# Kernel optimization log

Measured on AMD Instinct MI355X. Metric: run time of the kernel, lower is better.

Reference implementation:

```python
import jax, jax.numpy as jnp
import numpy as np

B, T, V, E, H, F, L = 128, 30, 10000, 512, 512, 4096, 2


def setup_inputs() -> dict:
    key = jax.random.key(0)
    ks = jax.random.split(key, 8)
    s = lambda n: np.float32(1.0 / np.sqrt(n))
    return {
        "vgg_fc7": jax.random.normal(ks[0], (B, F), jnp.float32),
        "xTokens": jax.random.randint(ks[1], (B, T), 0, V),
        "embedding": jax.random.normal(ks[2], (V, E), jnp.float32) * 0.1,
        "W_in": jax.random.normal(ks[3], (F, H), jnp.float32) * s(F),
        "b_in": jnp.zeros((H,), jnp.float32),
        # GRU params stacked over layers; layer0 input dim E == H so shapes match
        "Wu": jax.random.normal(ks[4], (L, E + H, H), jnp.float32) * s(E + H),
        "bu": jnp.zeros((L, H), jnp.float32),
        "Wr": jax.random.normal(ks[5], (L, E + H, H), jnp.float32) * s(E + H),
        "br": jnp.zeros((L, H), jnp.float32),
        "Wc": jax.random.normal(ks[6], (L, E + H, H), jnp.float32) * s(E + H),
        "bc": jnp.zeros((L, H), jnp.float32),
        "W_out": jax.random.normal(ks[7], (H, V), jnp.float32) * s(H),
        "b_out": jnp.zeros((V,), jnp.float32),
    }


def reference(vgg_fc7, xTokens, embedding, W_in, b_in, Wu, bu, Wr, br, Wc, bc, W_out, b_out):
    # initial hidden state = tanh(inputLayer(vgg_fc7)), replicated per layer
    h0 = jnp.tanh(vgg_fc7 @ W_in + b_in)            # [B, H]
    states0 = jnp.broadcast_to(h0, (L, B, H))
    x_emb = embedding[xTokens]                      # [B, T, E]

    def step(states, x_t):
        x = x_t                                     # [B, E]
        new = []
        for j in range(L):
            h = states[j]
            conc = jnp.concatenate([x, h], axis=1)              # [B, E+H]
            u = jax.nn.sigmoid(conc @ Wu[j] + bu[j])            # update gate
            r = jax.nn.sigmoid(conc @ Wr[j] + br[j])            # reset gate
            cand = jnp.tanh(jnp.concatenate([x, r * h], axis=1) @ Wc[j] + bc[j])
            h = u * h + (1.0 - u) * cand
            new.append(h)
            x = h
        logits_t = x @ W_out + b_out                # [B, V]
        return jnp.stack(new), logits_t

    final_state, logits = jax.lax.scan(step, states0, jnp.swapaxes(x_emb, 0, 1))
    logits = jnp.swapaxes(logits, 0, 1)             # [B, T, V]
    return logits, final_state
```

## Files before the change

kernel.cpp:

```cpp
#include <hip/hip_runtime.h>
#include <hip/hip_bf16.h>

#define B_   128
#define T_   30
#define V_   10000
#define E_   512
#define H_   512
#define F_   4096
#define L_   2
#define VPAD 10112

typedef __attribute__((ext_vector_type(4))) float f32x4;
typedef __attribute__((ext_vector_type(8))) __bf16 bf16x8;
typedef __attribute__((ext_vector_type(8))) unsigned short u16x8;

__device__ __forceinline__ unsigned short f2bf(float x){
    unsigned int u = __float_as_uint(x);
    unsigned int r = (u + 0x7FFFu + ((u >> 16) & 1u)) >> 16;
    return (unsigned short)r;
}

__global__ void __launch_bounds__(256) k_castWT(const float* __restrict__ W,
                                                unsigned short* __restrict__ WbT){
    __shared__ float tile[64][65];
    const int n0 = blockIdx.x * 64;
    const int k0 = blockIdx.y * 64;
    const int tid = threadIdx.x;
    for (int q = 0; q < 16; ++q){
        int idx = tid + q * 256;
        int kk = idx >> 6, nn = idx & 63;
        int n = n0 + nn;
        tile[kk][nn] = (n < V_) ? W[(size_t)(k0 + kk) * V_ + n] : 0.f;
    }
    __syncthreads();
    for (int q = 0; q < 16; ++q){
        int idx = tid + q * 256;
        int nn = idx >> 6, kk = idx & 63;
        WbT[(size_t)(n0 + nn) * 512 + k0 + kk] = f2bf(tile[kk][nn]);
    }
}

__global__ void __launch_bounds__(256) k_embed(const int* __restrict__ tok,
                                               const float* __restrict__ emb,
                                               float* __restrict__ xemb){
    int g  = blockIdx.x * 256 + threadIdx.x;
    int e4 = (g & 127) * 4;
    int b  = (g >> 7) & 127;
    int t  = g >> 14;
    int id = tok[b * T_ + t];
    const float4 v = *reinterpret_cast<const float4*>(emb + (size_t)id * E_ + e4);
    *reinterpret_cast<float4*>(xemb + ((size_t)t * B_ + b) * E_ + e4) = v;
}

__global__ void __launch_bounds__(256) k_h0p(const float* __restrict__ vgg,
                                             const float* __restrict__ Win,
                                             float* __restrict__ part){
    __shared__ float a[8][520];
    const int b0 = blockIdx.x * 8;
    const int fs = blockIdx.y;
    const int f0 = fs * 512;
    const int tid = threadIdx.x;
    for (int q = 0; q < 4; ++q){
        int idx = tid + q * 256;
        int r = idx >> 7, c4 = (idx & 127) * 4;
        *reinterpret_cast<float4*>(&a[r][c4]) =
            *reinterpret_cast<const float4*>(vgg + (size_t)(b0 + r) * F_ + f0 + c4);
    }
    __syncthreads();
    float acc[8][2];
    #pragma unroll
    for (int i = 0; i < 8; ++i){ acc[i][0] = 0.f; acc[i][1] = 0.f; }
    for (int f = 0; f < 512; f += 4){
        float w0a = Win[(size_t)(f0 + f    ) * H_ + tid];
        float w0b = Win[(size_t)(f0 + f    ) * H_ + tid + 256];
        float w1a = Win[(size_t)(f0 + f + 1) * H_ + tid];
        float w1b = Win[(size_t)(f0 + f + 1) * H_ + tid + 256];
        float w2a = Win[(size_t)(f0 + f + 2) * H_ + tid];
        float w2b = Win[(size_t)(f0 + f + 2) * H_ + tid + 256];
        float w3a = Win[(size_t)(f0 + f + 3) * H_ + tid];
        float w3b = Win[(size_t)(f0 + f + 3) * H_ + tid + 256];
        #pragma unroll
        for (int i = 0; i < 8; ++i){
            const float4 av = *reinterpret_cast<const float4*>(&a[i][f]);
            acc[i][0] += av.x * w0a + av.y * w1a + av.z * w2a + av.w * w3a;
            acc[i][1] += av.x * w0b + av.y * w1b + av.z * w2b + av.w * w3b;
        }
    }
    for (int i = 0; i < 8; ++i){
        part[((size_t)fs * B_ + b0 + i) * H_ + tid      ] = acc[i][0];
        part[((size_t)fs * B_ + b0 + i) * H_ + tid + 256] = acc[i][1];
    }
}

__global__ void __launch_bounds__(256) k_h0r(const float* __restrict__ part,
                                             const float* __restrict__ b_in,
                                             float* __restrict__ hbuf){
    int g  = blockIdx.x * 256 + threadIdx.x;
    int i4 = g * 4;
    float4 s = *reinterpret_cast<const float4*>(part + i4);
    for (int fs = 1; fs < 8; ++fs){
        const float4 p = *reinterpret_cast<const float4*>(part + (size_t)fs * 65536 + i4);
        s.x += p.x; s.y += p.y; s.z += p.z; s.w += p.w;
    }
    int h = i4 & 511;
    const float4 bi = *reinterpret_cast<const float4*>(b_in + h);
    float4 o;
    o.x = tanhf(s.x + bi.x); o.y = tanhf(s.y + bi.y);
    o.z = tanhf(s.z + bi.z); o.w = tanhf(s.w + bi.w);
    *reinterpret_cast<float4*>(hbuf + i4) = o;
    *reinterpret_cast<float4*>(hbuf + 131072 + i4) = o;
}

__global__ void __launch_bounds__(512) k_gates(const float* __restrict__ xsrc,
                                               const float* __restrict__ hsrc,
                                               const float* __restrict__ Wu,
                                               const float* __restrict__ Wr,
                                               const float* __restrict__ Wc,
                                               const float* __restrict__ bu,
                                               const float* __restrict__ br,
                                               const float* __restrict__ bc,
                                               float* __restrict__ ubuf,
                                               float* __restrict__ rbuf,
                                               float* __restrict__ cxbuf){
    __shared__ float a[32][132];
    const int bt = blockIdx.x;
    const int nt = blockIdx.y;
    const int sect = nt >> 3;
    const int b0 = bt * 32;
    const int tid = threadIdx.x;
    const int nl = tid & 63;
    const int bg = tid >> 6;
    const int ncol = (nt & 7) * 64 + nl;
    const float* W = (sect == 0) ? Wu : (sect == 1) ? Wr : Wc;
    float acc[4] = {0.f, 0.f, 0.f, 0.f};
    const int nch = (sect == 2) ? 4 : 8;
    for (int c = 0; c < nch; ++c){
        const float* src = (c < 4) ? xsrc : hsrc;
        const int kd = (c < 4) ? c * 128 : (c - 4) * 128;
        __syncthreads();
        {
            int idx = tid;
            #pragma unroll
            for (int q = 0; q < 2; ++q){
                int r = idx >> 5, c4 = (idx & 31) * 4;
                *reinterpret_cast<float4*>(&a[r][c4]) =
                    *reinterpret_cast<const float4*>(src + (size_t)(b0 + r) * 512 + kd + c4);
                idx += 512;
            }
        }
        __syncthreads();
        const int krow = c * 128;
        for (int kk = 0; kk < 128; kk += 4){
            const size_t wb = (size_t)(krow + kk) * 512 + ncol;
            const float w0 = W[wb];
            const float w1 = W[wb + 512];
            const float w2 = W[wb + 1024];
            const float w3 = W[wb + 1536];
            #pragma unroll
            for (int i = 0; i < 4; ++i){
                const float4 av = *reinterpret_cast<const float4*>(&a[bg * 4 + i][kk]);
                acc[i] += av.x * w0 + av.y * w1 + av.z * w2 + av.w * w3;
            }
        }
    }
    const float* bias = (sect == 0) ? bu : (sect == 1) ? br : bc;
    float* outp = (sect == 0) ? ubuf : (sect == 1) ? rbuf : cxbuf;
    const float bv = bias[ncol];
    #pragma unroll
    for (int i = 0; i < 4; ++i){
        const int b = b0 + bg * 4 + i;
        float v = acc[i] + bv;
        if (sect < 2) v = 1.f / (1.f + expf(-v));
        outp[(size_t)b * 512 + ncol] = v;
    }
}

__global__ void __launch_bounds__(256) k_cand(const float* __restrict__ hold,
                                              const float* __restrict__ rbuf,
                                              const float* __restrict__ ubuf,
                                              const float* __restrict__ cxbuf,
                                              const float* __restrict__ Wc,
                                              float* __restrict__ hnew,
                                              unsigned short* __restrict__ xs16,
                                              float* __restrict__ fsout,
                                              int t, int j){
    __shared__ float a[16][132];
    const int b0 = blockIdx.x * 16;
    const int nt = blockIdx.y;
    const int tid = threadIdx.x;
    const int nl = tid & 63;
    const int bg = tid >> 6;
    const int n = nt * 64 + nl;
    float acc[4] = {0.f, 0.f, 0.f, 0.f};
    for (int c = 0; c < 4; ++c){
        const int kd = c * 128;
        __syncthreads();
        {
            int idx = tid;
            #pragma unroll
            for (int q = 0; q < 2; ++q){
                int r = idx >> 5, c4 = (idx & 31) * 4;
                const float4 rv = *reinterpret_cast<const float4*>(rbuf + (size_t)(b0 + r) * 512 + kd + c4);
                const float4 hv = *reinterpret_cast<const float4*>(hold + (size_t)(b0 + r) * 512 + kd + c4);
                float4 p;
                p.x = rv.x * hv.x; p.y = rv.y * hv.y; p.z = rv.z * hv.z; p.w = rv.w * hv.w;
                *reinterpret_cast<float4*>(&a[r][c4]) = p;
                idx += 256;
            }
        }
        __syncthreads();
        for (int kk = 0; kk < 128; kk += 4){
            const size_t wb = (size_t)(512 + kd + kk) * 512 + n;
            const float w0 = Wc[wb];
            const float w1 = Wc[wb + 512];
            const float w2 = Wc[wb + 1024];
            const float w3 = Wc[wb + 1536];
            #pragma unroll
            for (int i = 0; i < 4; ++i){
                const float4 av = *reinterpret_cast<const float4*>(&a[bg * 4 + i][kk]);
                acc[i] += av.x * w0 + av.y * w1 + av.z * w2 + av.w * w3;
            }
        }
    }
    #pragma unroll
    for (int i = 0; i < 4; ++i){
        const int b = b0 + bg * 4 + i;
        const float cand = tanhf(cxbuf[(size_t)b * 512 + n] + acc[i]);
        const float u = ubuf[(size_t)b * 512 + n];
        const float hv = hold[(size_t)b * 512 + n];
        const float h2 = u * hv + (1.f - u) * cand;
        hnew[(size_t)b * 512 + n] = h2;
        if (j == 1) xs16[((size_t)t * B_ + b) * 512 + n] = f2bf(h2);
        if (t == T_ - 1) fsout[(size_t)j * 65536 + (size_t)b * 512 + n] = h2;
    }
}

__global__ void __launch_bounds__(256) k_logits(const unsigned short* __restrict__ xs16,
                                                const unsigned short* __restrict__ WbT,
                                                const float* __restrict__ b_out,
                                                float* __restrict__ out){
    __shared__ unsigned short al[128 * 72];
    __shared__ unsigned short bl[128 * 72];
    const int n0 = blockIdx.x * 128;
    const int t  = blockIdx.y;
    const int m0 = t * 128;
    const int tid = threadIdx.x;
    const int lane = tid & 63;
    const int wid = tid >> 6;
    const int wm = (wid >> 1) * 64;
    const int wn = (wid & 1) * 64;
    f32x4 acc[4][4];
    #pragma unroll
    for (int i = 0; i < 4; ++i)
        #pragma unroll
        for (int jj = 0; jj < 4; ++jj)
            acc[i][jj] = (f32x4){0.f, 0.f, 0.f, 0.f};

    for (int c = 0; c < 8; ++c){
        const int k0 = c * 64;
        __syncthreads();
        #pragma unroll
        for (int q = 0; q < 4; ++q){
            const int li = tid + q * 256;
            const int row = li >> 3;
            const int seg = li & 7;
            *reinterpret_cast<u16x8*>(&al[row * 72 + seg * 8]) =
                *reinterpret_cast<const u16x8*>(xs16 + (size_t)(m0 + row) * 512 + k0 + seg * 8);
            *reinterpret_cast<u16x8*>(&bl[row * 72 + seg * 8]) =
                *reinterpret_cast<const u16x8*>(WbT + (size_t)(n0 + row) * 512 + k0 + seg * 8);
        }
        __syncthreads();
        #pragma unroll
        for (int ks = 0; ks < 2; ++ks){
            bf16x8 af[4], bfr[4];
            #pragma unroll
            for (int f = 0; f < 4; ++f){
                af[f]  = *reinterpret_cast<const bf16x8*>(
                    &al[(wm + f * 16 + (lane & 15)) * 72 + ks * 32 + (lane >> 4) * 8]);
                bfr[f] = *reinterpret_cast<const bf16x8*>(
                    &bl[(wn + f * 16 + (lane & 15)) * 72 + ks * 32 + (lane >> 4) * 8]);
            }
            #pragma unroll
            for (int fm = 0; fm < 4; ++fm)
                #pragma unroll
                for (int fn = 0; fn < 4; ++fn)
                    acc[fm][fn] = __builtin_amdgcn_mfma_f32_16x16x32_bf16(
                        af[fm], bfr[fn], acc[fm][fn], 0, 0, 0);
        }
    }
    #pragma unroll
    for (int fm = 0; fm < 4; ++fm){
        #pragma unroll
        for (int fn = 0; fn < 4; ++fn){
            const int v = n0 + wn + fn * 16 + (lane & 15);
            if (v < V_){
                const float bo = b_out[v];
                #pragma unroll
                for (int mi = 0; mi < 4; ++mi){
                    const int b = wm + fm * 16 + (lane >> 4) * 4 + mi;
                    out[(size_t)b * (T_ * V_) + (size_t)t * V_ + v] = acc[fm][fn][mi] + bo;
                }
            }
        }
    }
}

extern "C" void kernel_launch(void* const* d_in, const int* in_sizes, int n_in,
                              void* d_out, int out_size, void* d_ws, size_t ws_size,
                              hipStream_t stream){
    const float* vgg  = (const float*)d_in[0];
    const int*   tok  = (const int*)  d_in[1];
    const float* emb  = (const float*)d_in[2];
    const float* Win  = (const float*)d_in[3];
    const float* bin  = (const float*)d_in[4];
    const float* Wu   = (const float*)d_in[5];
    const float* bu   = (const float*)d_in[6];
    const float* Wr   = (const float*)d_in[7];
    const float* br   = (const float*)d_in[8];
    const float* Wc   = (const float*)d_in[9];
    const float* bc   = (const float*)d_in[10];
    const float* Wout = (const float*)d_in[11];
    const float* bout = (const float*)d_in[12];
    float* out = (float*)d_out;

    float* ws    = (float*)d_ws;
    float* hbuf  = ws;
    float* ubuf  = ws + 262144;
    float* rbuf  = ws + 327680;
    float* cxbuf = ws + 393216;
    float* xemb  = ws + 458752;
    float* h0p   = ws + 2424832;
    unsigned short* xs16 = (unsigned short*)((char*)d_ws + 11796480);
    unsigned short* WbT  = (unsigned short*)((char*)d_ws + 11796480 + 3932160);

    k_castWT<<<dim3(158, 8), dim3(256), 0, stream>>>(Wout, WbT);
    k_embed<<<dim3(1920), dim3(256), 0, stream>>>(tok, emb, xemb);
    k_h0p<<<dim3(16, 8), dim3(256), 0, stream>>>(vgg, Win, h0p);
    k_h0r<<<dim3(64), dim3(256), 0, stream>>>(h0p, bin, hbuf);

    for (int t = 0; t < T_; ++t){
        const int rp = t & 1, wp = rp ^ 1;
        for (int j = 0; j < L_; ++j){
            const float* xsrc = (j == 0) ? (xemb + (size_t)t * 65536)
                                         : (hbuf + (size_t)wp * 65536);
            const float* hold = hbuf + (size_t)j * 131072 + (size_t)rp * 65536;
            float* hnew       = hbuf + (size_t)j * 131072 + (size_t)wp * 65536;
            const float* Wuj = Wu + (size_t)j * 524288;
            const float* Wrj = Wr + (size_t)j * 524288;
            const float* Wcj = Wc + (size_t)j * 524288;
            const float* buj = bu + (size_t)j * 512;
            const float* brj = br + (size_t)j * 512;
            const float* bcj = bc + (size_t)j * 512;
            k_gates<<<dim3(4, 24), dim3(512), 0, stream>>>(
                xsrc, hold, Wuj, Wrj, Wcj, buj, brj, bcj, ubuf, rbuf, cxbuf);
            k_cand<<<dim3(8, 8), dim3(256), 0, stream>>>(
                hold, rbuf, ubuf, cxbuf, Wcj, hnew, xs16, out + 38400000, t, j);
        }
    }
    k_logits<<<dim3(79, 30), dim3(256), 0, stream>>>(xs16, WbT, bout, out);
}
```

Measured before the change: 6.711 ms.

## Fuse GRU recurrence into persistent cooperative kernel with grid barriers and hoisted input GEMM

Replaces 120 per-step gate/candidate launches with one cooperative persistent kernel that syncs phases via a global atomic barrier. The layer-0 input projection for all timesteps is hoisted into one bf16 MFMA GEMM before the recurrence. Recurrent weights are repacked into a coalesced float4 layout. It removes launch overhead and the repeated x-part matmuls, but adds grid-barrier latency and bf16 rounding on the layer-0 input path.

```diff
diff --git a/kernel.cpp b/kernel.cpp
--- a/kernel.cpp
+++ b/kernel.cpp
@@ -40,16 +40,60 @@
     }
 }
 
-__global__ void __launch_bounds__(256) k_embed(const int* __restrict__ tok,
-                                               const float* __restrict__ emb,
-                                               float* __restrict__ xemb){
-    int g  = blockIdx.x * 256 + threadIdx.x;
-    int e4 = (g & 127) * 4;
-    int b  = (g >> 7) & 127;
-    int t  = g >> 14;
+__global__ void __launch_bounds__(256) k_castWxT(const float* __restrict__ src,
+                                                 unsigned short* __restrict__ dst){
+    __shared__ float tile[64][65];
+    const int n0 = blockIdx.x * 64;
+    const int k0 = blockIdx.y * 64;
+    const int tid = threadIdx.x;
+    for (int q = 0; q < 16; ++q){
+        int idx = tid + q * 256;
+        int kk = idx >> 6, nn = idx & 63;
+        tile[kk][nn] = src[(size_t)(k0 + kk) * 512 + n0 + nn];
+    }
+    __syncthreads();
+    for (int q = 0; q < 16; ++q){
+        int idx = tid + q * 256;
+        int nn = idx >> 6, kk = idx & 63;
+        dst[(size_t)(n0 + nn) * 512 + k0 + kk] = f2bf(tile[kk][nn]);
+    }
+}
+
+__global__ void __launch_bounds__(256) k_prepW(float* __restrict__ dst,
+                                               const float* __restrict__ srcA,
+                                               const float* __restrict__ srcB,
+                                               int koff, int Kq){
+    const int idx = blockIdx.x * 256 + threadIdx.x;
+    const int l = idx & 63;
+    const int gk = idx >> 6;
+    const int kq = gk % Kq;
+    const int g  = gk / Kq;
+    const int n = g * 64 + l;
+    const float* s = (n < 512) ? srcA : srcB;
+    const int nc = n & 511;
+    const int k = koff + kq * 4;
+    float4 v;
+    v.x = s[(size_t)(k    ) * 512 + nc];
+    v.y = s[(size_t)(k + 1) * 512 + nc];
+    v.z = s[(size_t)(k + 2) * 512 + nc];
+    v.w = s[(size_t)(k + 3) * 512 + nc];
+    *reinterpret_cast<float4*>(&dst[(size_t)idx * 4]) = v;
+}
+
+__global__ void __launch_bounds__(256) k_embed16(const int* __restrict__ tok,
+                                                 const float* __restrict__ emb,
+                                                 unsigned short* __restrict__ xe){
+    int g = blockIdx.x * 256 + threadIdx.x;
+    int e8 = (g & 63) * 8;
+    int b  = (g >> 6) & 127;
+    int t  = g >> 13;
     int id = tok[b * T_ + t];
-    const float4 v = *reinterpret_cast<const float4*>(emb + (size_t)id * E_ + e4);
-    *reinterpret_cast<float4*>(xemb + ((size_t)t * B_ + b) * E_ + e4) = v;
+    const float4 v0 = *reinterpret_cast<const float4*>(emb + (size_t)id * E_ + e8);
+    const float4 v1 = *reinterpret_cast<const float4*>(emb + (size_t)id * E_ + e8 + 4);
+    u16x8 o;
+    o[0] = f2bf(v0.x); o[1] = f2bf(v0.y); o[2] = f2bf(v0.z); o[3] = f2bf(v0.w);
+    o[4] = f2bf(v1.x); o[5] = f2bf(v1.y); o[6] = f2bf(v1.z); o[7] = f2bf(v1.w);
+    *reinterpret_cast<u16x8*>(&xe[((size_t)t * B_ + b) * 512 + e8]) = o;
 }
 
 __global__ void __launch_bounds__(256) k_h0p(const float* __restrict__ vgg,
@@ -94,7 +138,9 @@
 
 __global__ void __launch_bounds__(256) k_h0r(const float* __restrict__ part,
                                              const float* __restrict__ b_in,
-                                             float* __restrict__ hbuf){
+                                             float* __restrict__ h0a,
+                                             float* __restrict__ h1a,
+                                             unsigned* __restrict__ bar){
     int g  = blockIdx.x * 256 + threadIdx.x;
     int i4 = g * 4;
     float4 s = *reinterpret_cast<const float4*>(part + i4);
@@ -107,131 +153,245 @@
     float4 o;
     o.x = tanhf(s.x + bi.x); o.y = tanhf(s.y + bi.y);
     o.z = tanhf(s.z + bi.z); o.w = tanhf(s.w + bi.w);
-    *reinterpret_cast<float4*>(hbuf + i4) = o;
-    *reinterpret_cast<float4*>(hbuf + 131072 + i4) = o;
-}
-
-__global__ void __launch_bounds__(512) k_gates(const float* __restrict__ xsrc,
-                                               const float* __restrict__ hsrc,
-                                               const float* __restrict__ Wu,
-                                               const float* __restrict__ Wr,
-                                               const float* __restrict__ Wc,
-                                               const float* __restrict__ bu,
-                                               const float* __restrict__ br,
-                                               const float* __restrict__ bc,
-                                               float* __restrict__ ubuf,
-                                               float* __restrict__ rbuf,
-                                               float* __restrict__ cxbuf){
-    __shared__ float a[32][132];
-    const int bt = blockIdx.x;
-    const int nt = blockIdx.y;
-    const int sect = nt >> 3;
-    const int b0 = bt * 32;
+    *reinterpret_cast<float4*>(h0a + i4) = o;
+    *reinterpret_cast<float4*>(h1a + i4) = o;
+    if (blockIdx.x == 0 && threadIdx.x == 0){ bar[0] = 0u; bar[1] = 0u; }
+}
+
+__global__ void __launch_bounds__(256) k_gx(const unsigned short* __restrict__ xe,
+                                            const unsigned short* __restrict__ WxT,
+                                            const float* __restrict__ bu0,
+                                            const float* __restrict__ br0,
+                                            const float* __restrict__ bc0,
+                                            float* __restrict__ gx){
+    __shared__ unsigned short al[128 * 72];
+    __shared__ unsigned short bl[128 * 72];
+    const int n0 = blockIdx.x * 128;
+    const int m0 = blockIdx.y * 128;
     const int tid = threadIdx.x;
-    const int nl = tid & 63;
-    const int bg = tid >> 6;
-    const int ncol = (nt & 7) * 64 + nl;
-    const float* W = (sect == 0) ? Wu : (sect == 1) ? Wr : Wc;
-    float acc[4] = {0.f, 0.f, 0.f, 0.f};
-    const int nch = (sect == 2) ? 4 : 8;
-    for (int c = 0; c < nch; ++c){
-        const float* src = (c < 4) ? xsrc : hsrc;
-        const int kd = (c < 4) ? c * 128 : (c - 4) * 128;
+    const int lane = tid & 63;
+    const int wid = tid >> 6;
+    const int wm = (wid >> 1) * 64;
+    const int wn = (wid & 1) * 64;
+    f32x4 acc[4][4];
+    #pragma unroll
+    for (int i = 0; i < 4; ++i)
+        #pragma unroll
+        for (int jj = 0; jj < 4; ++jj)
+            acc[i][jj] = (f32x4){0.f, 0.f, 0.f, 0.f};
+
+    for (int c = 0; c < 8; ++c){
+        const int k0 = c * 64;
         __syncthreads();
+        #pragma unroll
+        for (int q = 0; q < 4; ++q){
+            const int li = tid + q * 256;
+            const int row = li >> 3;
+            const int seg = li & 7;
+            *reinterpret_cast<u16x8*>(&al[row * 72 + seg * 8]) =
+                *reinterpret_cast<const u16x8*>(xe + (size_t)(m0 + row) * 512 + k0 + seg * 8);
+            *reinterpret_cast<u16x8*>(&bl[row * 72 + seg * 8]) =
+                *reinterpret_cast<const u16x8*>(WxT + (size_t)(n0 + row) * 512 + k0 + seg * 8);
+        }
+        __syncthreads();
+        #pragma unroll
+        for (int ks = 0; ks < 2; ++ks){
+            bf16x8 af[4], bfr[4];
+            #pragma unroll
+            for (int f = 0; f < 4; ++f){
+                af[f]  = *reinterpret_cast<const bf16x8*>(
+                    &al[(wm + f * 16 + (lane & 15)) * 72 + ks * 32 + (lane >> 4) * 8]);
+                bfr[f] = *reinterpret_cast<const bf16x8*>(
+                    &bl[(wn + f * 16 + (lane & 15)) * 72 + ks * 32 + (lane >> 4) * 8]);
+            }
+            #pragma unroll
+            for (int fm = 0; fm < 4; ++fm)
+                #pragma unroll
+                for (int fn = 0; fn < 4; ++fn)
+                    acc[fm][fn] = __builtin_amdgcn_mfma_f32_16x16x32_bf16(
+                        af[fm], bfr[fn], acc[fm][fn], 0, 0, 0);
+        }
+    }
+    #pragma unroll
+    for (int fm = 0; fm < 4; ++fm){
+        #pragma unroll
+        for (int fn = 0; fn < 4; ++fn){
+            const int cl = n0 + wn + fn * 16 + (lane & 15);
+            const float bo = (cl < 512) ? bu0[cl] : (cl < 1024) ? br0[cl - 512] : bc0[cl - 1024];
+            #pragma unroll
+            for (int mi = 0; mi < 4; ++mi){
+                const int m = m0 + wm + fm * 16 + (lane >> 4) * 4 + mi;
+                gx[(size_t)m * 1536 + cl] = acc[fm][fn][mi] + bo;
+            }
+        }
+    }
+}
+
+struct RecurArgs {
+    const float* gx;
+    const float* Wg0; const float* Wc0; const float* Wg1; const float* Wc1;
+    const float* bu1; const float* br1; const float* bc1;
+    float* h0a; float* h0b; float* h1a; float* h1b;
+    float* ur0; float* ur1;
+    unsigned short* xs16;
+    float* fsout;
+    unsigned* bar;
+};
+
+__device__ __forceinline__ void gridbar(unsigned* bar, int target){
+    __syncthreads();
+    if (threadIdx.x == 0){
+        __threadfence();
+        unsigned arr = __hip_atomic_fetch_add(&bar[0], 1u, __ATOMIC_ACQ_REL,
+                                              __HIP_MEMORY_SCOPE_AGENT) + 1u;
+        if (arr == (unsigned)(256 * target)){
+            __hip_atomic_store(&bar[1], (unsigned)target, __ATOMIC_RELEASE,
+                               __HIP_MEMORY_SCOPE_AGENT);
+        } else {
+            while ((int)__hip_atomic_load(&bar[1], __ATOMIC_ACQUIRE,
+                                          __HIP_MEMORY_SCOPE_AGENT) < target){
+                __builtin_amdgcn_s_sleep(2);
+            }
+        }
+    }
+    __syncthreads();
+}
+
+template<int K>
+__device__ __forceinline__ float2 core(const float* __restrict__ Wp,
+                                       const float* as_, int n0, int lane, int w){
+    float a0a = 0.f, a0b = 0.f, a1a = 0.f, a1b = 0.f;
+    const float* bp = Wp + ((size_t)(n0 >> 6) * (K >> 2)) * 256 + lane * 4;
+    const float* ar0 = as_ + (w * 2 + 0) * K;
+    const float* ar1 = as_ + (w * 2 + 1) * K;
+    #pragma unroll 4
+    for (int kq = 0; kq < (K >> 2); ++kq){
+        const float4 bv  = *reinterpret_cast<const float4*>(bp + (size_t)kq * 256);
+        const float4 av0 = *reinterpret_cast<const float4*>(ar0 + kq * 4);
+        const float4 av1 = *reinterpret_cast<const float4*>(ar1 + kq * 4);
+        a0a = fmaf(av0.x, bv.x, a0a); a0b = fmaf(av0.y, bv.y, a0b);
+        a0a = fmaf(av0.z, bv.z, a0a); a0b = fmaf(av0.w, bv.w, a0b);
+        a1a = fmaf(av1.x, bv.x, a1a); a1b = fmaf(av1.y, bv.y, a1b);
+        a1a = fmaf(av1.z, bv.z, a1a); a1b = fmaf(av1.w, bv.w, a1b);
+    }
+    float2 r; r.x = a0a + a0b; r.y = a1a + a1b; return r;
+}
+
+__global__ void __launch_bounds__(256) k_recur(RecurArgs A){
+    __shared__ float as_[8192];
+    const int blk = blockIdx.x, tid = threadIdx.x;
+    const int lane = tid & 63, w = tid >> 6;
+    int gen = 0;
+    for (int t = 0; t < T_; ++t){
+        float* h0old = (t & 1) ? A.h0b : A.h0a;
+        float* h0new = (t & 1) ? A.h0a : A.h0b;
+        float* h1old = (t & 1) ? A.h1b : A.h1a;
+        float* h1new = (t & 1) ? A.h1a : A.h1b;
+        const float* gxt = A.gx + (size_t)t * 196608;
+
         {
-            int idx = tid;
-            #pragma unroll
-            for (int q = 0; q < 2; ++q){
-                int r = idx >> 5, c4 = (idx & 31) * 4;
-                *reinterpret_cast<float4*>(&a[r][c4]) =
-                    *reinterpret_cast<const float4*>(src + (size_t)(b0 + r) * 512 + kd + c4);
-                idx += 512;
-            }
-        }
-        __syncthreads();
-        const int krow = c * 128;
-        for (int kk = 0; kk < 128; kk += 4){
-            const size_t wb = (size_t)(krow + kk) * 512 + ncol;
-            const float w0 = W[wb];
-            const float w1 = W[wb + 512];
-            const float w2 = W[wb + 1024];
-            const float w3 = W[wb + 1536];
-            #pragma unroll
-            for (int i = 0; i < 4; ++i){
-                const float4 av = *reinterpret_cast<const float4*>(&a[bg * 4 + i][kk]);
-                acc[i] += av.x * w0 + av.y * w1 + av.z * w2 + av.w * w3;
-            }
-        }
-    }
-    const float* bias = (sect == 0) ? bu : (sect == 1) ? br : bc;
-    float* outp = (sect == 0) ? ubuf : (sect == 1) ? rbuf : cxbuf;
-    const float bv = bias[ncol];
-    #pragma unroll
-    for (int i = 0; i < 4; ++i){
-        const int b = b0 + bg * 4 + i;
-        float v = acc[i] + bv;
-        if (sect < 2) v = 1.f / (1.f + expf(-v));
-        outp[(size_t)b * 512 + ncol] = v;
-    }
-}
-
-__global__ void __launch_bounds__(256) k_cand(const float* __restrict__ hold,
-                                              const float* __restrict__ rbuf,
-                                              const float* __restrict__ ubuf,
-                                              const float* __restrict__ cxbuf,
-                                              const float* __restrict__ Wc,
-                                              float* __restrict__ hnew,
-                                              unsigned short* __restrict__ xs16,
-                                              float* __restrict__ fsout,
-                                              int t, int j){
-    __shared__ float a[16][132];
-    const int b0 = blockIdx.x * 16;
-    const int nt = blockIdx.y;
-    const int tid = threadIdx.x;
-    const int nl = tid & 63;
-    const int bg = tid >> 6;
-    const int n = nt * 64 + nl;
-    float acc[4] = {0.f, 0.f, 0.f, 0.f};
-    for (int c = 0; c < 4; ++c){
-        const int kd = c * 128;
-        __syncthreads();
+            const int m0 = (blk >> 4) * 8, n0 = (blk & 15) * 64;
+            for (int q = 0; q < 4; ++q){
+                int idx = tid + q * 256, r = idx >> 7, c4 = (idx & 127) << 2;
+                *reinterpret_cast<float4*>(&as_[r * 512 + c4]) =
+                    *reinterpret_cast<const float4*>(&h0old[(size_t)(m0 + r) * 512 + c4]);
+            }
+            __syncthreads();
+            float2 s = core<512>(A.Wg0, as_, n0, lane, w);
+            const int n = n0 + lane;
+            #pragma unroll
+            for (int i = 0; i < 2; ++i){
+                const int m = m0 + w * 2 + i;
+                float pre = ((i == 0) ? s.x : s.y) + gxt[(size_t)m * 1536 + n];
+                A.ur0[(size_t)m * 1024 + n] = 1.f / (1.f + __expf(-pre));
+            }
+        }
+        gridbar(A.bar, ++gen);
+
+        if (blk < 128){
+            const int m0 = (blk >> 3) * 8, n0 = (blk & 7) * 64;
+            for (int q = 0; q < 4; ++q){
+                int idx = tid + q * 256, r = idx >> 7, c4 = (idx & 127) << 2;
+                const float4 rv = *reinterpret_cast<const float4*>(
+                    &A.ur0[(size_t)(m0 + r) * 1024 + 512 + c4]);
+                const float4 hv = *reinterpret_cast<const float4*>(
+                    &h0old[(size_t)(m0 + r) * 512 + c4]);
+                float4 p; p.x = rv.x*hv.x; p.y = rv.y*hv.y; p.z = rv.z*hv.z; p.w = rv.w*hv.w;
+                *reinterpret_cast<float4*>(&as_[r * 512 + c4]) = p;
+            }
+            __syncthreads();
+            float2 s = core<512>(A.Wc0, as_, n0, lane, w);
+            const int n = n0 + lane;
+            #pragma unroll
+            for (int i = 0; i < 2; ++i){
+                const int m = m0 + w * 2 + i;
+                float cand = tanhf(((i == 0) ? s.x : s.y) + gxt[(size_t)m * 1536 + 1024 + n]);
+                float u = A.ur0[(size_t)m * 1024 + n];
+                float h = h0old[(size_t)m * 512 + n];
+                float h2 = u * h + (1.f - u) * cand;
+                h0new[(size_t)m * 512 + n] = h2;
+                if (t == T_ - 1) A.fsout[(size_t)m * 512 + n] = h2;
+            }
+        }
+        gridbar(A.bar, ++gen);
+
         {
-            int idx = tid;
-            #pragma unroll
-            for (int q = 0; q < 2; ++q){
-                int r = idx >> 5, c4 = (idx & 31) * 4;
-                const float4 rv = *reinterpret_cast<const float4*>(rbuf + (size_t)(b0 + r) * 512 + kd + c4);
-                const float4 hv = *reinterpret_cast<const float4*>(hold + (size_t)(b0 + r) * 512 + kd + c4);
-                float4 p;
-                p.x = rv.x * hv.x; p.y = rv.y * hv.y; p.z = rv.z * hv.z; p.w = rv.w * hv.w;
-                *reinterpret_cast<float4*>(&a[r][c4]) = p;
-                idx += 256;
-            }
-        }
-        __syncthreads();
-        for (int kk = 0; kk < 128; kk += 4){
-            const size_t wb = (size_t)(512 + kd + kk) * 512 + n;
-            const float w0 = Wc[wb];
-            const float w1 = Wc[wb + 512];
-            const float w2 = Wc[wb + 1024];
-            const float w3 = Wc[wb + 1536];
-            #pragma unroll
-            for (int i = 0; i < 4; ++i){
-                const float4 av = *reinterpret_cast<const float4*>(&a[bg * 4 + i][kk]);
-                acc[i] += av.x * w0 + av.y * w1 + av.z * w2 + av.w * w3;
-            }
-        }
-    }
-    #pragma unroll
-    for (int i = 0; i < 4; ++i){
-        const int b = b0 + bg * 4 + i;
-        const float cand = tanhf(cxbuf[(size_t)b * 512 + n] + acc[i]);
-        const float u = ubuf[(size_t)b * 512 + n];
-        const float hv = hold[(size_t)b * 512 + n];
-        const float h2 = u * hv + (1.f - u) * cand;
-        hnew[(size_t)b * 512 + n] = h2;
-        if (j == 1) xs16[((size_t)t * B_ + b) * 512 + n] = f2bf(h2);
-        if (t == T_ - 1) fsout[(size_t)j * 65536 + (size_t)b * 512 + n] = h2;
+            const int m0 = (blk >> 4) * 8, n0 = (blk & 15) * 64;
+            for (int q = 0; q < 8; ++q){
+                int idx = tid + q * 256, r = idx >> 8, c4 = (idx & 255) << 2;
+                float4 v;
+                if (c4 < 512) v = *reinterpret_cast<const float4*>(
+                                    &h0new[(size_t)(m0 + r) * 512 + c4]);
+                else          v = *reinterpret_cast<const float4*>(
+                                    &h1old[(size_t)(m0 + r) * 512 + (c4 - 512)]);
+                *reinterpret_cast<float4*>(&as_[r * 1024 + c4]) = v;
+            }
+            __syncthreads();
+            float2 s = core<1024>(A.Wg1, as_, n0, lane, w);
+            const int n = n0 + lane;
+            const float bias = (n < 512) ? A.bu1[n] : A.br1[n - 512];
+            #pragma unroll
+            for (int i = 0; i < 2; ++i){
+                const int m = m0 + w * 2 + i;
+                float pre = ((i == 0) ? s.x : s.y) + bias;
+                A.ur1[(size_t)m * 1024 + n] = 1.f / (1.f + __expf(-pre));
+            }
+        }
+        gridbar(A.bar, ++gen);
+
+        if (blk < 128){
+            const int m0 = (blk >> 3) * 8, n0 = (blk & 7) * 64;
+            for (int q = 0; q < 8; ++q){
+                int idx = tid + q * 256, r = idx >> 8, c4 = (idx & 255) << 2;
+                float4 v;
+                if (c4 < 512){
+                    v = *reinterpret_cast<const float4*>(&h0new[(size_t)(m0 + r) * 512 + c4]);
+                } else {
+                    const float4 rv = *reinterpret_cast<const float4*>(
+                        &A.ur1[(size_t)(m0 + r) * 1024 + 512 + (c4 - 512)]);
+                    const float4 hv = *reinterpret_cast<const float4*>(
+                        &h1old[(size_t)(m0 + r) * 512 + (c4 - 512)]);
+                    v.x = rv.x*hv.x; v.y = rv.y*hv.y; v.z = rv.z*hv.z; v.w = rv.w*hv.w;
+                }
+                *reinterpret_cast<float4*>(&as_[r * 1024 + c4]) = v;
+            }
+            __syncthreads();
+            float2 s = core<1024>(A.Wc1, as_, n0, lane, w);
+            const int n = n0 + lane;
+            const float bias = A.bc1[n];
+            #pragma unroll
+            for (int i = 0; i < 2; ++i){
+                const int m = m0 + w * 2 + i;
+                float cand = tanhf(((i == 0) ? s.x : s.y) + bias);
+                float u = A.ur1[(size_t)m * 1024 + n];
+                float h = h1old[(size_t)m * 512 + n];
+                float h2 = u * h + (1.f - u) * cand;
+                h1new[(size_t)m * 512 + n] = h2;
+                A.xs16[((size_t)t * B_ + m) * 512 + n] = f2bf(h2);
+                if (t == T_ - 1) A.fsout[65536 + (size_t)m * 512 + n] = h2;
+            }
+        }
+        gridbar(A.bar, ++gen);
     }
 }
 
@@ -323,39 +483,50 @@
     const float* bout = (const float*)d_in[12];
     float* out = (float*)d_out;
 
-    float* ws    = (float*)d_ws;
-    float* hbuf  = ws;
-    float* ubuf  = ws + 262144;
-    float* rbuf  = ws + 327680;
-    float* cxbuf = ws + 393216;
-    float* xemb  = ws + 458752;
-    float* h0p   = ws + 2424832;
-    unsigned short* xs16 = (unsigned short*)((char*)d_ws + 11796480);
-    unsigned short* WbT  = (unsigned short*)((char*)d_ws + 11796480 + 3932160);
+    float* ws = (float*)d_ws;
+    float* h0a  = ws;
+    float* h0b  = ws + 65536;
+    float* h1a  = ws + 131072;
+    float* h1b  = ws + 196608;
+    float* ur0  = ws + 262144;
+    float* ur1  = ws + 393216;
+    float* gx   = ws + 524288;
+    float* h0p  = ws + 6422528;
+    float* Wg0  = ws + 6946816;
+    float* Wc0  = ws + 7471104;
+    float* Wg1  = ws + 7733248;
+    float* Wc1  = ws + 8781824;
+    unsigned* bar = (unsigned*)(ws + 9306112);
+    unsigned short* xs16   = (unsigned short*)((char*)d_ws + 37224960);
+    unsigned short* WbT    = (unsigned short*)((char*)d_ws + 41157120);
+    unsigned short* xemb16 = (unsigned short*)((char*)d_ws + 51511808);
+    unsigned short* WxT    = (unsigned short*)((char*)d_ws + 55443968);
+
+    const float* Wu0 = Wu, *Wu1 = Wu + 524288;
+    const float* Wr0 = Wr, *Wr1 = Wr + 524288;
+    const float* Wc0s = Wc, *Wc1s = Wc + 524288;
 
     k_castWT<<<dim3(158, 8), dim3(256), 0, stream>>>(Wout, WbT);
-    k_embed<<<dim3(1920), dim3(256), 0, stream>>>(tok, emb, xemb);
+    k_castWxT<<<dim3(8, 8), dim3(256), 0, stream>>>(Wu0,  WxT);
+    k_castWxT<<<dim3(8, 8), dim3(256), 0, stream>>>(Wr0,  WxT + 262144);
+    k_castWxT<<<dim3(8, 8), dim3(256), 0, stream>>>(Wc0s, WxT + 524288);
+    k_embed16<<<dim3(960), dim3(256), 0, stream>>>(tok, emb, xemb16);
+    k_prepW<<<dim3(512),  dim3(256), 0, stream>>>(Wg0, Wu0,  Wr0,  512, 128);
+    k_prepW<<<dim3(256),  dim3(256), 0, stream>>>(Wc0, Wc0s, Wc0s, 512, 128);
+    k_prepW<<<dim3(1024), dim3(256), 0, stream>>>(Wg1, Wu1,  Wr1,  0,   256);
+    k_prepW<<<dim3(512),  dim3(256), 0, stream>>>(Wc1, Wc1s, Wc1s, 0,   256);
     k_h0p<<<dim3(16, 8), dim3(256), 0, stream>>>(vgg, Win, h0p);
-    k_h0r<<<dim3(64), dim3(256), 0, stream>>>(h0p, bin, hbuf);
-
-    for (int t = 0; t < T_; ++t){
-        const int rp = t & 1, wp = rp ^ 1;
-        for (int j = 0; j < L_; ++j){
-            const float* xsrc = (j == 0) ? (xemb + (size_t)t * 65536)
-                                         : (hbuf + (size_t)wp * 65536);
-            const float* hold = hbuf + (size_t)j * 131072 + (size_t)rp * 65536;
-            float* hnew       = hbuf + (size_t)j * 131072 + (size_t)wp * 65536;
-            const float* Wuj = Wu + (size_t)j * 524288;
-            const float* Wrj = Wr + (size_t)j * 524288;
-            const float* Wcj = Wc + (size_t)j * 524288;
-            const float* buj = bu + (size_t)j * 512;
-            const float* brj = br + (size_t)j * 512;
-            const float* bcj = bc + (size_t)j * 512;
-            k_gates<<<dim3(4, 24), dim3(512), 0, stream>>>(
-                xsrc, hold, Wuj, Wrj, Wcj, buj, brj, bcj, ubuf, rbuf, cxbuf);
-            k_cand<<<dim3(8, 8), dim3(256), 0, stream>>>(
-                hold, rbuf, ubuf, cxbuf, Wcj, hnew, xs16, out + 38400000, t, j);
-        }
-    }
+    k_h0r<<<dim3(64), dim3(256), 0, stream>>>(h0p, bin, h0a, h1a, bar);
+    k_gx<<<dim3(12, 30), dim3(256), 0, stream>>>(xemb16, WxT, bu, br, bc, gx);
+
+    RecurArgs ra;
+    ra.gx = gx; ra.Wg0 = Wg0; ra.Wc0 = Wc0; ra.Wg1 = Wg1; ra.Wc1 = Wc1;
+    ra.bu1 = bu + 512; ra.br1 = br + 512; ra.bc1 = bc + 512;
+    ra.h0a = h0a; ra.h0b = h0b; ra.h1a = h1a; ra.h1b = h1b;
+    ra.ur0 = ur0; ra.ur1 = ur1;
+    ra.xs16 = xs16; ra.fsout = out + 38400000; ra.bar = bar;
+    void* args[] = { &ra };
+    hipLaunchCooperativeKernel((const void*)k_recur, dim3(256), dim3(256), args, 0, stream);
+
     k_logits<<<dim3(79, 30), dim3(256), 0, stream>>>(xs16, WbT, bout, out);
 }
```

After: 14.37 ms. +114.1%, slower.
